# Optimization experiments

Hardware: AMD Instinct MI355X
Metric: run time of the kernel (lower is better)

## Reference

```python
import jax, jax.numpy as jnp
import numpy as np

B, S, E, H = 4, 2048, 1024, 16
D = E // H  # head_size = 64


def setup_inputs() -> dict:
    key = jax.random.key(0)
    ks = jax.random.split(key, 8)
    s = 1.0 / np.sqrt(E)
    return {
        "values": jax.random.normal(ks[0], (B, S, E), jnp.float32),
        "keys": jax.random.normal(ks[1], (B, S, E), jnp.float32),
        "queries": jax.random.normal(ks[2], (B, S, E), jnp.float32),
        "Wv": jax.random.normal(ks[3], (E, E), jnp.float32) * s,
        "Wk": jax.random.normal(ks[4], (E, E), jnp.float32) * s,
        "Wq": jax.random.normal(ks[5], (E, E), jnp.float32) * s,
        "Wo": jax.random.normal(ks[6], (E, E), jnp.float32) * s,
        "bo": jax.random.normal(ks[7], (E,), jnp.float32) * s,
    }


def reference(values, keys, queries, Wv, Wk, Wq, Wo, bo):
    # torch Linear: y = x @ W.T
    k = (keys @ Wk.T).reshape(B, S, H, D).transpose(0, 2, 1, 3)    # [B,H,S,D]
    q = (queries @ Wq.T).reshape(B, S, H, D).transpose(0, 2, 1, 3)
    v = (values @ Wv.T).reshape(B, S, H, D).transpose(0, 2, 1, 3)
    dot = jnp.einsum('bhqd,bhkd->bhqk', q, k)                      # raw logits
    # NOTE: softmax BEFORE scaling (faithful to original module)
    probs = jax.nn.softmax(dot, axis=-1) / jnp.sqrt(jnp.float32(D))
    out = jnp.einsum('bhqk,bhkd->bhqd', probs, v)                  # [B,H,S,D]
    out = out.transpose(0, 2, 1, 3).reshape(B, S, E)
    return out @ Wo.T + bo
```

## Files before the change

### kernel.cpp

```cpp
#include <hip/hip_runtime.h>
#include <stdint.h>

#define NB 4
#define NS 2048
#define NE 1024
#define NH 16
#define ND 64

typedef __attribute__((ext_vector_type(8))) short short8;
typedef __attribute__((ext_vector_type(2))) float f32x2;
typedef __attribute__((ext_vector_type(4))) float f32x4;
typedef __attribute__((ext_vector_type(8))) float f32x8;
typedef __attribute__((ext_vector_type(16))) float f32x16;
typedef __attribute__((ext_vector_type(4))) unsigned short us4;
typedef __attribute__((ext_vector_type(4))) unsigned int u32x4;
typedef __attribute__((ext_vector_type(2))) __bf16 bf16x2;

#define LOG2E 1.4426950408889634f

__device__ __forceinline__ unsigned short f2bf(float f) {
    return __builtin_bit_cast(unsigned short, static_cast<__bf16>(f));
}
__device__ __forceinline__ unsigned int packbf(float lo, float hi_) {
    f32x2 v; v[0] = lo; v[1] = hi_;
    return __builtin_bit_cast(unsigned int, __builtin_convertvector(v, bf16x2));
}
__device__ __forceinline__ float exp2n(float x) {
    float y;
    asm("v_exp_f32 %0, %1" : "=v"(y) : "v"(x));
    return y;
}
__device__ __forceinline__ void gl_lds16(const void* g, void* l) {
    __builtin_amdgcn_global_load_lds(
        (const __attribute__((address_space(1))) unsigned int*)g,
        (__attribute__((address_space(3))) unsigned int*)l, 16, 0, 0);
}

__global__ __launch_bounds__(256) void cvt_all_kernel(
    const float* __restrict__ w0, const float* __restrict__ w1,
    const float* __restrict__ w2, const float* __restrict__ w3,
    const float* __restrict__ x0, const float* __restrict__ x1,
    const float* __restrict__ x2,
    unsigned short* __restrict__ dw0, unsigned short* __restrict__ dw1,
    unsigned short* __restrict__ dw2, unsigned short* __restrict__ dw3,
    unsigned short* __restrict__ dx0, unsigned short* __restrict__ dx1,
    unsigned short* __restrict__ dx2) {
    const int bid = blockIdx.x;
    const float* src;
    unsigned short* dst;
    int idx;
    float scl = 1.0f;
    if (bid < 4096) {
        const int g = bid >> 10;
        src = g == 0 ? w0 : g == 1 ? w1 : g == 2 ? w2 : w3;
        dst = g == 0 ? dw0 : g == 1 ? dw1 : g == 2 ? dw2 : dw3;
        if (g == 2) scl = LOG2E;
        idx = ((bid & 1023) * 256 + threadIdx.x) * 4;
    } else {
        const int b2 = bid - 4096;
        const int g = b2 >> 13;
        src = g == 0 ? x0 : g == 1 ? x1 : x2;
        dst = g == 0 ? dx0 : g == 1 ? dx1 : dx2;
        idx = ((b2 & 8191) * 256 + threadIdx.x) * 4;
    }
    f32x4 f = *(const f32x4*)(src + idx);
    us4 o;
#pragma unroll
    for (int j = 0; j < 4; ++j) o[j] = f2bf(f[j] * scl);
    *(us4*)(dst + idx) = o;
}

struct GemmArgs {
    const unsigned short *a0, *a1, *a2;
    const unsigned short *w0, *w1, *w2;
    void *c0, *c1, *c2;
    const float* bias;
};

template<int OUT_SEL>
__global__ __launch_bounds__(256) void gemm_glds(GemmArgs args) {
    __shared__ __align__(16) unsigned short As[2][4096];
    __shared__ __align__(16) unsigned short Bs[2][4096];
    const int tid = threadIdx.x;
    const int bm = blockIdx.x, bn = blockIdx.y, z = blockIdx.z;
    const unsigned short* Ab = z == 0 ? args.a0 : z == 1 ? args.a1 : args.a2;
    const unsigned short* Wb = z == 0 ? args.w0 : z == 1 ? args.w1 : args.w2;
    void* Cp               = z == 0 ? args.c0 : z == 1 ? args.c1 : args.c2;
    const int lane = tid & 63, wid = tid >> 6;
    const int lr = lane & 15, lg = lane >> 4;
    const int wr = wid >> 1, wc = wid & 1;

    const size_t aoff = (size_t)(bm * 128 + (tid >> 2)) * 1024 + (tid & 3) * 8;
    const size_t boff = (size_t)(bn * 128 + (tid >> 2)) * 1024 + (tid & 3) * 8;

    f32x4 acc[4][4];
#pragma unroll
    for (int a = 0; a < 4; ++a)
#pragma unroll
        for (int b = 0; b < 4; ++b) acc[a][b] = (f32x4){0.f, 0.f, 0.f, 0.f};

#define STAGE(buf, kk) { \
    gl_lds16(Ab + aoff + (kk),             &As[buf][tid * 8]); \
    gl_lds16(Ab + aoff + 64 * 1024 + (kk), &As[buf][2048 + tid * 8]); \
    gl_lds16(Wb + boff + (kk),             &Bs[buf][tid * 8]); \
    gl_lds16(Wb + boff + 64 * 1024 + (kk), &Bs[buf][2048 + tid * 8]); }

    STAGE(0, 0)
    __syncthreads();
    int cur = 0;
    for (int k0 = 0; k0 < 1024; k0 += 32) {
        if (k0 + 32 < 1024) STAGE(cur ^ 1, k0 + 32)
        short8 af[4], bfr[4];
#pragma unroll
        for (int mi = 0; mi < 4; ++mi)
            af[mi] = *(const short8*)&As[cur][(wr * 64 + mi * 16 + lr) * 32 + lg * 8];
#pragma unroll
        for (int ni = 0; ni < 4; ++ni)
            bfr[ni] = *(const short8*)&Bs[cur][(wc * 64 + ni * 16 + lr) * 32 + lg * 8];
#pragma unroll
        for (int mi = 0; mi < 4; ++mi)
#pragma unroll
            for (int ni = 0; ni < 4; ++ni)
                acc[mi][ni] = __builtin_amdgcn_mfma_f32_16x16x32_bf16(af[mi], bfr[ni], acc[mi][ni], 0, 0, 0);
        __syncthreads();
        cur ^= 1;
    }
#undef STAGE

#pragma unroll
    for (int mi = 0; mi < 4; ++mi) {
#pragma unroll
        for (int ni = 0; ni < 4; ++ni) {
            const int n = bn * 128 + wc * 64 + ni * 16 + lr;
            if (OUT_SEL == 1) {
#pragma unroll
                for (int i = 0; i < 4; ++i) {
                    const int m = bm * 128 + wr * 64 + mi * 16 + lg * 4 + i;
                    ((float*)Cp)[(size_t)m * 1024 + n] = acc[mi][ni][i] + args.bias[n];
                }
            } else if (z == 2) {
                const int m0 = bm * 128 + wr * 64 + mi * 16 + lg * 4;
                const int b = m0 >> 11, s0 = m0 & 2047;
                const int h = n >> 6, d = n & 63;
                us4 pk;
#pragma unroll
                for (int i = 0; i < 4; ++i) pk[i] = f2bf(acc[mi][ni][i]);
                const size_t idx = ((((size_t)b * NH + h) * (NS / 64) + (s0 >> 6)) * ND + d) * 64 + (s0 & 63);
                *(us4*)&((unsigned short*)Cp)[idx] = pk;
            } else {
#pragma unroll
                for (int i = 0; i < 4; ++i) {
                    const int m = bm * 128 + wr * 64 + mi * 16 + lg * 4 + i;
                    const int b = m >> 11, s = m & 2047, h = n >> 6, d = n & 63;
                    ((unsigned short*)Cp)[(((size_t)b * NH + h) * NS + s) * ND + d] = f2bf(acc[mi][ni][i]);
                }
            }
        }
    }
}

__global__ __launch_bounds__(256, 4) void attn_kernel(const unsigned short* __restrict__ q,
                                                      const unsigned short* __restrict__ k,
                                                      const unsigned short* __restrict__ vtt,
                                                      unsigned short* __restrict__ o) {
    __shared__ unsigned short Kl[2][64][72];
    __shared__ unsigned short Vl[2][64][72];
    const int tid = threadIdx.x;
    const int lane = tid & 63, wid = tid >> 6;
    const int l31 = lane & 31, hi = lane >> 5;
    const int bh = blockIdx.y;
    const int qw = blockIdx.x * 128 + wid * 32;
    const size_t base = (size_t)bh * NS * ND;

    short8 qf[4];
    {
        const unsigned short* qp = q + base + (size_t)(qw + l31) * ND + 8 * hi;
#pragma unroll
        for (int m = 0; m < 4; ++m) qf[m] = *(const short8*)(qp + 16 * m);
    }

    float l_run = 0.f;
    f32x16 oa0, oa1, fz;
#pragma unroll
    for (int i = 0; i < 16; ++i) { oa0[i] = 0.f; oa1[i] = 0.f; fz[i] = 0.f; }

    const int strow = tid >> 2, stcol = (tid & 3) * 16;
    const unsigned short* ks = k   + base + tid * 16;
    const unsigned short* vs = vtt + base + tid * 16;

    short8 kr0 = *(const short8*)(ks);
    short8 kr1 = *(const short8*)(ks + 8);
    short8 vr0 = *(const short8*)(vs);
    short8 vr1 = *(const short8*)(vs + 8);

    for (int t = 0; t < NS / 64; ++t) {
        const int buf = t & 1;
        *(short8*)&Kl[buf][strow][stcol]     = kr0;
        *(short8*)&Kl[buf][strow][stcol + 8] = kr1;
        *(short8*)&Vl[buf][strow][stcol]     = vr0;
        *(short8*)&Vl[buf][strow][stcol + 8] = vr1;

        if (t + 1 < NS / 64) {
            const unsigned short* ks2 = ks + (size_t)(t + 1) * 64 * ND;
            const unsigned short* vs2 = vs + (size_t)(t + 1) * 64 * ND;
            kr0 = *(const short8*)(ks2);
            kr1 = *(const short8*)(ks2 + 8);
            vr0 = *(const short8*)(vs2);
            vr1 = *(const short8*)(vs2 + 8);
        }

        __syncthreads();

        f32x16 st0, st1;
        __builtin_amdgcn_s_setprio(1);
        {
            short8 kf;
            kf = *(const short8*)&Kl[buf][l31][8 * hi];
            st0 = __builtin_amdgcn_mfma_f32_32x32x16_bf16(kf, qf[0], fz, 0, 0, 0);
            kf = *(const short8*)&Kl[buf][l31][16 + 8 * hi];
            st0 = __builtin_amdgcn_mfma_f32_32x32x16_bf16(kf, qf[1], st0, 0, 0, 0);
            kf = *(const short8*)&Kl[buf][l31][32 + 8 * hi];
            st0 = __builtin_amdgcn_mfma_f32_32x32x16_bf16(kf, qf[2], st0, 0, 0, 0);
            kf = *(const short8*)&Kl[buf][l31][48 + 8 * hi];
            st0 = __builtin_amdgcn_mfma_f32_32x32x16_bf16(kf, qf[3], st0, 0, 0, 0);
            kf = *(const short8*)&Kl[buf][32 + l31][8 * hi];
            st1 = __builtin_amdgcn_mfma_f32_32x32x16_bf16(kf, qf[0], fz, 0, 0, 0);
            kf = *(const short8*)&Kl[buf][32 + l31][16 + 8 * hi];
            st1 = __builtin_amdgcn_mfma_f32_32x32x16_bf16(kf, qf[1], st1, 0, 0, 0);
            kf = *(const short8*)&Kl[buf][32 + l31][32 + 8 * hi];
            st1 = __builtin_amdgcn_mfma_f32_32x32x16_bf16(kf, qf[2], st1, 0, 0, 0);
            kf = *(const short8*)&Kl[buf][32 + l31][48 + 8 * hi];
            st1 = __builtin_amdgcn_mfma_f32_32x32x16_bf16(kf, qf[3], st1, 0, 0, 0);
        }
        __builtin_amdgcn_s_setprio(0);

        st0 = st0 - 64.0f;
        st1 = st1 - 64.0f;
#pragma unroll
        for (int i = 0; i < 16; ++i) st0[i] = exp2n(st0[i]);
#pragma unroll
        for (int i = 0; i < 16; ++i) st1[i] = exp2n(st1[i]);
        {
            f32x16 sv = st0 + st1;
            f32x8 s8 = __builtin_shufflevector(sv, sv, 0, 1, 2, 3, 4, 5, 6, 7)
                     + __builtin_shufflevector(sv, sv, 8, 9, 10, 11, 12, 13, 14, 15);
            f32x4 s4 = __builtin_shufflevector(s8, s8, 0, 1, 2, 3)
                     + __builtin_shufflevector(s8, s8, 4, 5, 6, 7);
            f32x2 s2 = __builtin_shufflevector(s4, s4, 0, 1)
                     + __builtin_shufflevector(s4, s4, 2, 3);
            float rs = s2[0] + s2[1];
            rs += __shfl_xor(rs, 32, 64);
            l_run += rs;
        }

        short8 pf0, pf1, pf2, pf3;
#define MKPF(PF, SV, RB) { \
        unsigned int wa = packbf(SV[RB + 0], SV[RB + 1]); \
        unsigned int wb = packbf(SV[RB + 2], SV[RB + 3]); \
        unsigned int wc = packbf(SV[RB + 4], SV[RB + 5]); \
        unsigned int wd = packbf(SV[RB + 6], SV[RB + 7]); \
        asm("v_permlane32_swap_b32 %0, %1" : "+v"(wa), "+v"(wc)); \
        asm("v_permlane32_swap_b32 %0, %1" : "+v"(wb), "+v"(wd)); \
        u32x4 pw; pw[0] = wa; pw[1] = wb; pw[2] = wc; pw[3] = wd; \
        PF = __builtin_bit_cast(short8, pw); }
        MKPF(pf0, st0, 0)
        MKPF(pf1, st0, 8)
        MKPF(pf2, st1, 0)
        MKPF(pf3, st1, 8)
#undef MKPF

        __builtin_amdgcn_s_setprio(1);
        {
            short8 vf;
            vf = *(const short8*)&Vl[buf][l31][8 * hi];
            oa0 = __builtin_amdgcn_mfma_f32_32x32x16_bf16(vf, pf0, oa0, 0, 0, 0);
            vf = *(const short8*)&Vl[buf][l31][16 + 8 * hi];
            oa0 = __builtin_amdgcn_mfma_f32_32x32x16_bf16(vf, pf1, oa0, 0, 0, 0);
            vf = *(const short8*)&Vl[buf][l31][32 + 8 * hi];
            oa0 = __builtin_amdgcn_mfma_f32_32x32x16_bf16(vf, pf2, oa0, 0, 0, 0);
            vf = *(const short8*)&Vl[buf][l31][48 + 8 * hi];
            oa0 = __builtin_amdgcn_mfma_f32_32x32x16_bf16(vf, pf3, oa0, 0, 0, 0);
            vf = *(const short8*)&Vl[buf][32 + l31][8 * hi];
            oa1 = __builtin_amdgcn_mfma_f32_32x32x16_bf16(vf, pf0, oa1, 0, 0, 0);
            vf = *(const short8*)&Vl[buf][32 + l31][16 + 8 * hi];
            oa1 = __builtin_amdgcn_mfma_f32_32x32x16_bf16(vf, pf1, oa1, 0, 0, 0);
            vf = *(const short8*)&Vl[buf][32 + l31][32 + 8 * hi];
            oa1 = __builtin_amdgcn_mfma_f32_32x32x16_bf16(vf, pf2, oa1, 0, 0, 0);
            vf = *(const short8*)&Vl[buf][32 + l31][48 + 8 * hi];
            oa1 = __builtin_amdgcn_mfma_f32_32x32x16_bf16(vf, pf3, oa1, 0, 0, 0);
        }
        __builtin_amdgcn_s_setprio(0);
    }

    const int b = bh >> 4, h = bh & 15;
    const float scl = 0.125f / l_run;
    unsigned short* op = o + (((size_t)b * NS + (qw + l31)) * NH + h) * ND;
#pragma unroll
    for (int rq = 0; rq < 4; ++rq) {
        us4 p0, p1;
#pragma unroll
        for (int i = 0; i < 4; ++i) {
            p0[i] = f2bf(oa0[4 * rq + i] * scl);
            p1[i] = f2bf(oa1[4 * rq + i] * scl);
        }
        *(us4*)&op[8 * rq + 4 * hi]      = p0;
        *(us4*)&op[32 + 8 * rq + 4 * hi] = p1;
    }
}

extern "C" void kernel_launch(void* const* d_in, const int* in_sizes, int n_in,
                              void* d_out, int out_size, void* d_ws, size_t ws_size,
                              hipStream_t stream) {
    (void)in_sizes; (void)n_in; (void)out_size; (void)ws_size;
    const float* values  = (const float*)d_in[0];
    const float* keys    = (const float*)d_in[1];
    const float* queries = (const float*)d_in[2];
    const float* Wv = (const float*)d_in[3];
    const float* Wk = (const float*)d_in[4];
    const float* Wq = (const float*)d_in[5];
    const float* Wo = (const float*)d_in[6];
    const float* bo = (const float*)d_in[7];

    uint8_t* ws = (uint8_t*)d_ws;
    const size_t MB = (size_t)1 << 20;
    unsigned short* wvb = (unsigned short*)(ws + 0 * MB);
    unsigned short* wkb = (unsigned short*)(ws + 2 * MB);
    unsigned short* wqb = (unsigned short*)(ws + 4 * MB);
    unsigned short* wob = (unsigned short*)(ws + 6 * MB);
    unsigned short* qb  = (unsigned short*)(ws + 8 * MB);
    unsigned short* kb  = (unsigned short*)(ws + 24 * MB);
    unsigned short* vtb = (unsigned short*)(ws + 40 * MB);
    unsigned short* ab  = (unsigned short*)(ws + 56 * MB);

    unsigned short* aq = (unsigned short*)d_out;
    unsigned short* ak = (unsigned short*)d_out + 8388608;
    unsigned short* av = ab;

    cvt_all_kernel<<<28672, 256, 0, stream>>>(Wv, Wk, Wq, Wo, queries, keys, values,
                                              wvb, wkb, wqb, wob, aq, ak, av);

    GemmArgs gqkv;
    gqkv.a0 = aq;  gqkv.a1 = ak;  gqkv.a2 = av;
    gqkv.w0 = wqb; gqkv.w1 = wkb; gqkv.w2 = wvb;
    gqkv.c0 = qb;  gqkv.c1 = kb;  gqkv.c2 = vtb;
    gqkv.bias = nullptr;
    gemm_glds<0><<<dim3(64, 8, 3), 256, 0, stream>>>(gqkv);

    attn_kernel<<<dim3(16, 64), 256, 0, stream>>>(qb, kb, vtb, ab);

    GemmArgs ge;
    ge.a0 = ge.a1 = ge.a2 = ab;
    ge.w0 = ge.w1 = ge.w2 = wob;
    ge.c0 = ge.c1 = ge.c2 = d_out;
    ge.bias = bo;
    gemm_glds<1><<<dim3(64, 8, 1), 256, 0, stream>>>(ge);
}
```

Baseline: 216.8 us.

## Stage K/V tiles via direct global-to-LDS loads with XOR-swizzled layout

Result: no change. 215.0 us (-0.8%).

```diff
diff --git a/kernel.cpp b/kernel.cpp
--- a/kernel.cpp
+++ b/kernel.cpp
@@ -163,8 +163,8 @@
                                                       const unsigned short* __restrict__ k,
                                                       const unsigned short* __restrict__ vtt,
                                                       unsigned short* __restrict__ o) {
-    __shared__ unsigned short Kl[2][64][72];
-    __shared__ unsigned short Vl[2][64][72];
+    __shared__ __align__(16) unsigned short Kl[2][4096];
+    __shared__ __align__(16) unsigned short Vl[2][4096];
     const int tid = threadIdx.x;
     const int lane = tid & 63, wid = tid >> 6;
     const int l31 = lane & 31, hi = lane >> 5;
@@ -184,52 +184,50 @@
 #pragma unroll
     for (int i = 0; i < 16; ++i) { oa0[i] = 0.f; oa1[i] = 0.f; fz[i] = 0.f; }
 
-    const int strow = tid >> 2, stcol = (tid & 3) * 16;
-    const unsigned short* ks = k   + base + tid * 16;
-    const unsigned short* vs = vtt + base + tid * 16;
-
-    short8 kr0 = *(const short8*)(ks);
-    short8 kr1 = *(const short8*)(ks + 8);
-    short8 vr0 = *(const short8*)(vs);
-    short8 vr1 = *(const short8*)(vs + 8);
-
+    const int g0 = wid * 128 + lane, g1 = g0 + 64;
+    const int r0 = g0 >> 3, c0 = ((g0 & 7) ^ (r0 & 7)) * 8;
+    const int r1 = g1 >> 3, c1 = ((g1 & 7) ^ (r1 & 7)) * 8;
+    const unsigned short* ks0 = k   + base + r0 * 64 + c0;
+    const unsigned short* ks1 = k   + base + r1 * 64 + c1;
+    const unsigned short* vs0 = vtt + base + r0 * 64 + c0;
+    const unsigned short* vs1 = vtt + base + r1 * 64 + c1;
+    const int ld0 = wid * 1024, ld1 = wid * 1024 + 512;
+
+#define STAGE(buf, t) { \
+    gl_lds16(ks0 + (size_t)(t) * 4096, &Kl[buf][ld0]); \
+    gl_lds16(ks1 + (size_t)(t) * 4096, &Kl[buf][ld1]); \
+    gl_lds16(vs0 + (size_t)(t) * 4096, &Vl[buf][ld0]); \
+    gl_lds16(vs1 + (size_t)(t) * 4096, &Vl[buf][ld1]); }
+
+    const int xr = (l31 & 7);
+    const int rA = l31 * 64, rB = (32 + l31) * 64;
+#define SW(c) ((((c) + hi) ^ xr) << 3)
+
+    STAGE(0, 0)
+    __syncthreads();
     for (int t = 0; t < NS / 64; ++t) {
         const int buf = t & 1;
-        *(short8*)&Kl[buf][strow][stcol]     = kr0;
-        *(short8*)&Kl[buf][strow][stcol + 8] = kr1;
-        *(short8*)&Vl[buf][strow][stcol]     = vr0;
-        *(short8*)&Vl[buf][strow][stcol + 8] = vr1;
-
-        if (t + 1 < NS / 64) {
-            const unsigned short* ks2 = ks + (size_t)(t + 1) * 64 * ND;
-            const unsigned short* vs2 = vs + (size_t)(t + 1) * 64 * ND;
-            kr0 = *(const short8*)(ks2);
-            kr1 = *(const short8*)(ks2 + 8);
-            vr0 = *(const short8*)(vs2);
-            vr1 = *(const short8*)(vs2 + 8);
-        }
-
-        __syncthreads();
+        if (t + 1 < NS / 64) STAGE(buf ^ 1, t + 1)
 
         f32x16 st0, st1;
         __builtin_amdgcn_s_setprio(1);
         {
             short8 kf;
-            kf = *(const short8*)&Kl[buf][l31][8 * hi];
+            kf = *(const short8*)&Kl[buf][rA + SW(0)];
             st0 = __builtin_amdgcn_mfma_f32_32x32x16_bf16(kf, qf[0], fz, 0, 0, 0);
-            kf = *(const short8*)&Kl[buf][l31][16 + 8 * hi];
+            kf = *(const short8*)&Kl[buf][rA + SW(2)];
             st0 = __builtin_amdgcn_mfma_f32_32x32x16_bf16(kf, qf[1], st0, 0, 0, 0);
-            kf = *(const short8*)&Kl[buf][l31][32 + 8 * hi];
+            kf = *(const short8*)&Kl[buf][rA + SW(4)];
             st0 = __builtin_amdgcn_mfma_f32_32x32x16_bf16(kf, qf[2], st0, 0, 0, 0);
-            kf = *(const short8*)&Kl[buf][l31][48 + 8 * hi];
+            kf = *(const short8*)&Kl[buf][rA + SW(6)];
             st0 = __builtin_amdgcn_mfma_f32_32x32x16_bf16(kf, qf[3], st0, 0, 0, 0);
-            kf = *(const short8*)&Kl[buf][32 + l31][8 * hi];
+            kf = *(const short8*)&Kl[buf][rB + SW(0)];
             st1 = __builtin_amdgcn_mfma_f32_32x32x16_bf16(kf, qf[0], fz, 0, 0, 0);
-            kf = *(const short8*)&Kl[buf][32 + l31][16 + 8 * hi];
+            kf = *(const short8*)&Kl[buf][rB + SW(2)];
             st1 = __builtin_amdgcn_mfma_f32_32x32x16_bf16(kf, qf[1], st1, 0, 0, 0);
-            kf = *(const short8*)&Kl[buf][32 + l31][32 + 8 * hi];
+            kf = *(const short8*)&Kl[buf][rB + SW(4)];
             st1 = __builtin_amdgcn_mfma_f32_32x32x16_bf16(kf, qf[2], st1, 0, 0, 0);
-            kf = *(const short8*)&Kl[buf][32 + l31][48 + 8 * hi];
+            kf = *(const short8*)&Kl[buf][rB + SW(6)];
             st1 = __builtin_amdgcn_mfma_f32_32x32x16_bf16(kf, qf[3], st1, 0, 0, 0);
         }
         __builtin_amdgcn_s_setprio(0);
@@ -272,25 +270,29 @@
         __builtin_amdgcn_s_setprio(1);
         {
             short8 vf;
-            vf = *(const short8*)&Vl[buf][l31][8 * hi];
+            vf = *(const short8*)&Vl[buf][rA + SW(0)];
             oa0 = __builtin_amdgcn_mfma_f32_32x32x16_bf16(vf, pf0, oa0, 0, 0, 0);
-            vf = *(const short8*)&Vl[buf][l31][16 + 8 * hi];
+            vf = *(const short8*)&Vl[buf][rA + SW(2)];
             oa0 = __builtin_amdgcn_mfma_f32_32x32x16_bf16(vf, pf1, oa0, 0, 0, 0);
-            vf = *(const short8*)&Vl[buf][l31][32 + 8 * hi];
+            vf = *(const short8*)&Vl[buf][rA + SW(4)];
             oa0 = __builtin_amdgcn_mfma_f32_32x32x16_bf16(vf, pf2, oa0, 0, 0, 0);
-            vf = *(const short8*)&Vl[buf][l31][48 + 8 * hi];
+            vf = *(const short8*)&Vl[buf][rA + SW(6)];
             oa0 = __builtin_amdgcn_mfma_f32_32x32x16_bf16(vf, pf3, oa0, 0, 0, 0);
-            vf = *(const short8*)&Vl[buf][32 + l31][8 * hi];
+            vf = *(const short8*)&Vl[buf][rB + SW(0)];
             oa1 = __builtin_amdgcn_mfma_f32_32x32x16_bf16(vf, pf0, oa1, 0, 0, 0);
-            vf = *(const short8*)&Vl[buf][32 + l31][16 + 8 * hi];
+            vf = *(const short8*)&Vl[buf][rB + SW(2)];
             oa1 = __builtin_amdgcn_mfma_f32_32x32x16_bf16(vf, pf1, oa1, 0, 0, 0);
-            vf = *(const short8*)&Vl[buf][32 + l31][32 + 8 * hi];
+            vf = *(const short8*)&Vl[buf][rB + SW(4)];
             oa1 = __builtin_amdgcn_mfma_f32_32x32x16_bf16(vf, pf2, oa1, 0, 0, 0);
-            vf = *(const short8*)&Vl[buf][32 + l31][48 + 8 * hi];
+            vf = *(const short8*)&Vl[buf][rB + SW(6)];
             oa1 = __builtin_amdgcn_mfma_f32_32x32x16_bf16(vf, pf3, oa1, 0, 0, 0);
         }
         __builtin_amdgcn_s_setprio(0);
-    }
+
+        __syncthreads();
+    }
+#undef STAGE
+#undef SW
 
     const int b = bh >> 4, h = bh & 15;
     const float scl = 0.125f / l_run;
```

## Fuse fp32-to-bf16 activation conversion into QKV projection GEMM A-tile loads

Applied to the files above, without the earlier changes.

Result: faster. 205.6 us, median of 2 (-5.2%).

```diff
diff --git a/kernel.cpp b/kernel.cpp
--- a/kernel.cpp
+++ b/kernel.cpp
@@ -36,56 +36,136 @@
         (__attribute__((address_space(3))) unsigned int*)l, 16, 0, 0);
 }
 
-__global__ __launch_bounds__(256) void cvt_all_kernel(
-    const float* __restrict__ w0, const float* __restrict__ w1,
-    const float* __restrict__ w2, const float* __restrict__ w3,
-    const float* __restrict__ x0, const float* __restrict__ x1,
-    const float* __restrict__ x2,
-    unsigned short* __restrict__ dw0, unsigned short* __restrict__ dw1,
-    unsigned short* __restrict__ dw2, unsigned short* __restrict__ dw3,
-    unsigned short* __restrict__ dx0, unsigned short* __restrict__ dx1,
-    unsigned short* __restrict__ dx2) {
-    const int bid = blockIdx.x;
-    const float* src;
-    unsigned short* dst;
-    int idx;
-    float scl = 1.0f;
-    if (bid < 4096) {
-        const int g = bid >> 10;
-        src = g == 0 ? w0 : g == 1 ? w1 : g == 2 ? w2 : w3;
-        dst = g == 0 ? dw0 : g == 1 ? dw1 : g == 2 ? dw2 : dw3;
-        if (g == 2) scl = LOG2E;
-        idx = ((bid & 1023) * 256 + threadIdx.x) * 4;
-    } else {
-        const int b2 = bid - 4096;
-        const int g = b2 >> 13;
-        src = g == 0 ? x0 : g == 1 ? x1 : x2;
-        dst = g == 0 ? dx0 : g == 1 ? dx1 : dx2;
-        idx = ((b2 & 8191) * 256 + threadIdx.x) * 4;
-    }
-    f32x4 f = *(const f32x4*)(src + idx);
+__global__ __launch_bounds__(256) void cvt_w4_kernel(const float* __restrict__ w0,
+                                                     const float* __restrict__ w1,
+                                                     const float* __restrict__ w2,
+                                                     const float* __restrict__ w3,
+                                                     unsigned short* __restrict__ d0,
+                                                     unsigned short* __restrict__ d1,
+                                                     unsigned short* __restrict__ d2,
+                                                     unsigned short* __restrict__ d3) {
+    const int g = blockIdx.x >> 10;
+    const float* src = g == 0 ? w0 : g == 1 ? w1 : g == 2 ? w2 : w3;
+    unsigned short* dst = g == 0 ? d0 : g == 1 ? d1 : g == 2 ? d2 : d3;
+    const float scl = (g == 2) ? LOG2E : 1.0f;
+    const int i = ((blockIdx.x & 1023) * 256 + threadIdx.x) * 4;
+    f32x4 f = *(const f32x4*)(src + i);
     us4 o;
 #pragma unroll
     for (int j = 0; j < 4; ++j) o[j] = f2bf(f[j] * scl);
-    *(us4*)(dst + idx) = o;
-}
-
-struct GemmArgs {
-    const unsigned short *a0, *a1, *a2;
+    *(us4*)(dst + i) = o;
+}
+
+struct HybArgs {
+    const float *a0, *a1, *a2;
     const unsigned short *w0, *w1, *w2;
     void *c0, *c1, *c2;
-    const float* bias;
 };
 
-template<int OUT_SEL>
-__global__ __launch_bounds__(256) void gemm_glds(GemmArgs args) {
+__global__ __launch_bounds__(256) void gemm_hyb(HybArgs args) {
+    __shared__ unsigned short As[2][128][40];
+    __shared__ __align__(16) unsigned short Bs[2][4096];
+    const int tid = threadIdx.x;
+    const int bm = blockIdx.x, bn = blockIdx.y, z = blockIdx.z;
+    const float* Ab          = z == 0 ? args.a0 : z == 1 ? args.a1 : args.a2;
+    const unsigned short* Wb = z == 0 ? args.w0 : z == 1 ? args.w1 : args.w2;
+    void* Cp                 = z == 0 ? args.c0 : z == 1 ? args.c1 : args.c2;
+    const int lane = tid & 63, wid = tid >> 6;
+    const int lr = lane & 15, lg = lane >> 4;
+    const int wr = wid >> 1, wc = wid & 1;
+    const int srow = tid >> 1, shalf = tid & 1;
+
+    const float* apF = Ab + (size_t)(bm * 128 + srow) * 1024 + shalf * 16;
+    const size_t boff = (size_t)(bn * 128 + (tid >> 2)) * 1024 + (tid & 3) * 8;
+
+    f32x4 acc[4][4];
+#pragma unroll
+    for (int a = 0; a < 4; ++a)
+#pragma unroll
+        for (int b = 0; b < 4; ++b) acc[a][b] = (f32x4){0.f, 0.f, 0.f, 0.f};
+
+#define STAGE_W(buf, kk) { \
+    gl_lds16(Wb + boff + (kk),             &Bs[buf][tid * 8]); \
+    gl_lds16(Wb + boff + 64 * 1024 + (kk), &Bs[buf][2048 + tid * 8]); }
+#define LOAD_A(kk) { \
+    pa0 = *(const f32x4*)(apF + (kk)); \
+    pa1 = *(const f32x4*)(apF + (kk) + 4); \
+    pa2 = *(const f32x4*)(apF + (kk) + 8); \
+    pa3 = *(const f32x4*)(apF + (kk) + 12); }
+#define WRITE_A(buf) { \
+    short8 p0, p1; \
+    for (int j = 0; j < 4; ++j) { \
+        p0[j] = (short)f2bf(pa0[j]); p0[j + 4] = (short)f2bf(pa1[j]); \
+        p1[j] = (short)f2bf(pa2[j]); p1[j + 4] = (short)f2bf(pa3[j]); } \
+    *(short8*)&As[buf][srow][shalf * 16]     = p0; \
+    *(short8*)&As[buf][srow][shalf * 16 + 8] = p1; }
+
+    f32x4 pa0, pa1, pa2, pa3;
+    LOAD_A(0)
+    STAGE_W(0, 0)
+    WRITE_A(0)
+    __syncthreads();
+    int cur = 0;
+    for (int k0 = 0; k0 < 1024; k0 += 32) {
+        const int last = (k0 + 32 >= 1024);
+        if (!last) {
+            STAGE_W(cur ^ 1, k0 + 32)
+            LOAD_A(k0 + 32)
+        }
+        short8 af[4], bfr[4];
+#pragma unroll
+        for (int mi = 0; mi < 4; ++mi)
+            af[mi] = *(const short8*)&As[cur][wr * 64 + mi * 16 + lr][lg * 8];
+#pragma unroll
+        for (int ni = 0; ni < 4; ++ni)
+            bfr[ni] = *(const short8*)&Bs[cur][(wc * 64 + ni * 16 + lr) * 32 + lg * 8];
+#pragma unroll
+        for (int mi = 0; mi < 4; ++mi)
+#pragma unroll
+            for (int ni = 0; ni < 4; ++ni)
+                acc[mi][ni] = __builtin_amdgcn_mfma_f32_16x16x32_bf16(af[mi], bfr[ni], acc[mi][ni], 0, 0, 0);
+        if (!last) WRITE_A(cur ^ 1)
+        __syncthreads();
+        cur ^= 1;
+    }
+#undef STAGE_W
+#undef LOAD_A
+#undef WRITE_A
+
+#pragma unroll
+    for (int mi = 0; mi < 4; ++mi) {
+#pragma unroll
+        for (int ni = 0; ni < 4; ++ni) {
+            const int n = bn * 128 + wc * 64 + ni * 16 + lr;
+            if (z == 2) {
+                const int m0 = bm * 128 + wr * 64 + mi * 16 + lg * 4;
+                const int b = m0 >> 11, s0 = m0 & 2047;
+                const int h = n >> 6, d = n & 63;
+                us4 pk;
+#pragma unroll
+                for (int i = 0; i < 4; ++i) pk[i] = f2bf(acc[mi][ni][i]);
+                const size_t idx = ((((size_t)b * NH + h) * (NS / 64) + (s0 >> 6)) * ND + d) * 64 + (s0 & 63);
+                *(us4*)&((unsigned short*)Cp)[idx] = pk;
+            } else {
+#pragma unroll
+                for (int i = 0; i < 4; ++i) {
+                    const int m = bm * 128 + wr * 64 + mi * 16 + lg * 4 + i;
+                    const int b = m >> 11, s = m & 2047, h = n >> 6, d = n & 63;
+                    ((unsigned short*)Cp)[(((size_t)b * NH + h) * NS + s) * ND + d] = f2bf(acc[mi][ni][i]);
+                }
+            }
+        }
+    }
+}
+
+__global__ __launch_bounds__(256) void gemm_glds(const unsigned short* __restrict__ Ab,
+                                                 const unsigned short* __restrict__ Wb,
+                                                 float* __restrict__ Cp,
+                                                 const float* __restrict__ bias) {
     __shared__ __align__(16) unsigned short As[2][4096];
     __shared__ __align__(16) unsigned short Bs[2][4096];
     const int tid = threadIdx.x;
-    const int bm = blockIdx.x, bn = blockIdx.y, z = blockIdx.z;
-    const unsigned short* Ab = z == 0 ? args.a0 : z == 1 ? args.a1 : args.a2;
-    const unsigned short* Wb = z == 0 ? args.w0 : z == 1 ? args.w1 : args.w2;
-    void* Cp               = z == 0 ? args.c0 : z == 1 ? args.c1 : args.c2;
+    const int bm = blockIdx.x, bn = blockIdx.y;
     const int lane = tid & 63, wid = tid >> 6;
     const int lr = lane & 15, lg = lane >> 4;
     const int wr = wid >> 1, wc = wid & 1;
@@ -132,28 +212,10 @@
 #pragma unroll
         for (int ni = 0; ni < 4; ++ni) {
             const int n = bn * 128 + wc * 64 + ni * 16 + lr;
-            if (OUT_SEL == 1) {
-#pragma unroll
-                for (int i = 0; i < 4; ++i) {
-                    const int m = bm * 128 + wr * 64 + mi * 16 + lg * 4 + i;
-                    ((float*)Cp)[(size_t)m * 1024 + n] = acc[mi][ni][i] + args.bias[n];
-                }
-            } else if (z == 2) {
-                const int m0 = bm * 128 + wr * 64 + mi * 16 + lg * 4;
-                const int b = m0 >> 11, s0 = m0 & 2047;
-                const int h = n >> 6, d = n & 63;
-                us4 pk;
-#pragma unroll
-                for (int i = 0; i < 4; ++i) pk[i] = f2bf(acc[mi][ni][i]);
-                const size_t idx = ((((size_t)b * NH + h) * (NS / 64) + (s0 >> 6)) * ND + d) * 64 + (s0 & 63);
-                *(us4*)&((unsigned short*)Cp)[idx] = pk;
-            } else {
-#pragma unroll
-                for (int i = 0; i < 4; ++i) {
-                    const int m = bm * 128 + wr * 64 + mi * 16 + lg * 4 + i;
-                    const int b = m >> 11, s = m & 2047, h = n >> 6, d = n & 63;
-                    ((unsigned short*)Cp)[(((size_t)b * NH + h) * NS + s) * ND + d] = f2bf(acc[mi][ni][i]);
-                }
+#pragma unroll
+            for (int i = 0; i < 4; ++i) {
+                const int m = bm * 128 + wr * 64 + mi * 16 + lg * 4 + i;
+                Cp[(size_t)m * 1024 + n] = acc[mi][ni][i] + bias[n];
             }
         }
     }
@@ -332,26 +394,15 @@
     unsigned short* vtb = (unsigned short*)(ws + 40 * MB);
     unsigned short* ab  = (unsigned short*)(ws + 56 * MB);
 
-    unsigned short* aq = (unsigned short*)d_out;
-    unsigned short* ak = (unsigned short*)d_out + 8388608;
-    unsigned short* av = ab;
-
-    cvt_all_kernel<<<28672, 256, 0, stream>>>(Wv, Wk, Wq, Wo, queries, keys, values,
-                                              wvb, wkb, wqb, wob, aq, ak, av);
-
-    GemmArgs gqkv;
-    gqkv.a0 = aq;  gqkv.a1 = ak;  gqkv.a2 = av;
-    gqkv.w0 = wqb; gqkv.w1 = wkb; gqkv.w2 = wvb;
-    gqkv.c0 = qb;  gqkv.c1 = kb;  gqkv.c2 = vtb;
-    gqkv.bias = nullptr;
-    gemm_glds<0><<<dim3(64, 8, 3), 256, 0, stream>>>(gqkv);
+    cvt_w4_kernel<<<4096, 256, 0, stream>>>(Wv, Wk, Wq, Wo, wvb, wkb, wqb, wob);
+
+    HybArgs hq;
+    hq.a0 = queries; hq.a1 = keys; hq.a2 = values;
+    hq.w0 = wqb;     hq.w1 = wkb; hq.w2 = wvb;
+    hq.c0 = qb;      hq.c1 = kb;  hq.c2 = vtb;
+    gemm_hyb<<<dim3(64, 8, 3), 256, 0, stream>>>(hq);
 
     attn_kernel<<<dim3(16, 64), 256, 0, stream>>>(qb, kb, vtb, ab);
 
-    GemmArgs ge;
-    ge.a0 = ge.a1 = ge.a2 = ab;
-    ge.w0 = ge.w1 = ge.w2 = wob;
-    ge.c0 = ge.c1 = ge.c2 = d_out;
-    ge.bias = bo;
-    gemm_glds<1><<<dim3(64, 8, 1), 256, 0, stream>>>(ge);
-}
+    gemm_glds<<<dim3(64, 8), 256, 0, stream>>>(ab, wob, (float*)d_out, bo);
+}
```
